# Kernel tuning notes

Hardware: AMD Instinct MI355X
Metric: run time of the kernel (lower is better)

Reference implementation:

```python
import jax, jax.numpy as jnp
import numpy as np

N, M, D, H = 256, 1024, 512, 512


def setup_inputs() -> dict:
    key = jax.random.key(0)
    k1, k2, k3, k4 = jax.random.split(key, 4)
    scale = 1.0 / np.sqrt(D)
    return {
        "embeddings": jax.random.normal(k1, (N, D), dtype=jnp.float32),
        "support_tensors": jax.random.normal(k2, (M, D), dtype=jnp.float32),
        "W1": jax.random.normal(k3, (D, H), dtype=jnp.float32) * scale,
        "b1": jnp.zeros((H,), dtype=jnp.float32),
        "W2": jax.random.normal(k4, (H, 1), dtype=jnp.float32) * (1.0 / np.sqrt(H)),
        "b2": jnp.zeros((1,), dtype=jnp.float32),
    }


def reference(embeddings, support_tensors, W1, b1, W2, b2):
    # SupportLayer.call: tile queries x support set into all N*M pairs,
    # apply pairwise kernel (siamese head: sigmoid(MLP(|a - b|))),
    # reshape back to similarity matrix [N, M].
    # Broadcasting replaces the explicit tf.tile / reshape.
    diff = jnp.abs(embeddings[:, None, :] - support_tensors[None, :, :])  # [N, M, D]
    h = jax.nn.relu(jnp.einsum("nmd,dh->nmh", diff, W1) + b1)             # [N, M, H]
    logits = jnp.einsum("nmh,ho->nmo", h, W2)[..., 0] + b2[0]             # [N, M]
    return jax.nn.sigmoid(logits)
```

## Files before the change

### kernel.cpp

```cpp
#include <hip/hip_runtime.h>
#include <hip/hip_bf16.h>

#define N_Q 256
#define M_S 1024
#define DD 512
#define HH 512

typedef __attribute__((ext_vector_type(8))) short short8;
typedef __attribute__((ext_vector_type(8))) __bf16 bf16x8;
typedef __attribute__((ext_vector_type(16))) float f32x16;
typedef __attribute__((ext_vector_type(2))) __bf16 bf16x2;

union U8 { short8 s; bf16x8 b; };

__device__ __forceinline__ unsigned short f2bf(float f) {
  unsigned int u = __float_as_uint(f);
  u += 0x7FFFu + ((u >> 16) & 1u);
  return (unsigned short)(u >> 16);
}

__device__ __forceinline__ short8 pack8(const float* d) {
#if defined(__has_builtin) && __has_builtin(__builtin_amdgcn_cvt_pk_bf16_f32)
  short8 r;
#pragma unroll
  for (int i = 0; i < 4; ++i) {
    union { bf16x2 v; short s[2]; } u;
    u.v = __builtin_amdgcn_cvt_pk_bf16_f32(d[2 * i], d[2 * i + 1]);
    r[2 * i] = u.s[0];
    r[2 * i + 1] = u.s[1];
  }
  return r;
#else
  short8 r;
#pragma unroll
  for (int i = 0; i < 8; ++i) r[i] = (short)f2bf(d[i]);
  return r;
#endif
}

__device__ __forceinline__ short8 packdiff(float4 e0, float4 e1, float4 s0, float4 s1) {
  float d[8];
  d[0] = fabsf(e0.x - s0.x); d[1] = fabsf(e0.y - s0.y);
  d[2] = fabsf(e0.z - s0.z); d[3] = fabsf(e0.w - s0.w);
  d[4] = fabsf(e1.x - s1.x); d[5] = fabsf(e1.y - s1.y);
  d[6] = fabsf(e1.z - s1.z); d[7] = fabsf(e1.w - s1.w);
  return pack8(d);
}

__global__ __launch_bounds__(512) void prep_w1s(const float* __restrict__ W1,
                                                unsigned short* __restrict__ w1s) {
  const int f = blockIdx.x;
  const int kc = f >> 4, h32 = f & 15;
  const int l = threadIdx.x & 63, j = threadIdx.x >> 6;
  const int h = h32 * 32 + (l & 31);
  const int k = kc * 16 + (l >> 5) * 8 + j;
  w1s[f * 512 + l * 8 + j] = f2bf(W1[k * HH + h]);
}

__global__ __launch_bounds__(256, 2) void support_kernel(
    const float* __restrict__ emb, const float* __restrict__ sup,
    const unsigned short* __restrict__ w1s, const float* __restrict__ b1,
    const float* __restrict__ W2, const float* __restrict__ b2,
    float* __restrict__ out) {
  __shared__ short As[64 * 512];

  const int tid = threadIdx.x;
  const int lane = tid & 63;
  const int wid = tid >> 6;
  const int l31 = lane & 31;
  const int khalf = lane >> 5;

  const int m0 = blockIdx.x * 16;
  const int n0 = blockIdx.y * 4;

  {
    const int c = tid & 63;
    const int pg = tid >> 6;
    const float* e = emb + (n0 + pg) * DD + c * 8;
    const float4 e0 = *(const float4*)e;
    const float4 e1 = *(const float4*)(e + 4);
    const float* sp = sup + m0 * DD + c * 8;
#pragma unroll
    for (int j = 0; j < 16; ++j) {
      const float4 s0 = *(const float4*)(sp + j * DD);
      const float4 s1 = *(const float4*)(sp + j * DD + 4);
      const int p = pg * 16 + j;
      *(short8*)&As[p * 512 + ((c ^ (j & 7)) * 8)] = packdiff(e0, e1, s0, s1);
    }
  }
  __syncthreads();

  const unsigned short* bb = w1s + (wid * 4) * 512 + lane * 8;
  const int ar0 = l31 * 512;
  const int ar1 = (32 + l31) * 512;
  const int ax = l31 & 7;

  f32x16 acc[2][4] = {};
  U8 a[2][2], b[2][4];

#pragma unroll
  for (int tj = 0; tj < 4; ++tj) b[0][tj].s = *(const short8*)(bb + tj * 512);
  {
    const int cc = (khalf ^ ax) * 8;
    a[0][0].s = *(const short8*)&As[ar0 + cc];
    a[0][1].s = *(const short8*)&As[ar1 + cc];
  }

#pragma unroll
  for (int kc = 0; kc < 32; ++kc) {
    const int cur = kc & 1, nxt = cur ^ 1;
    if (kc < 31) {
      const unsigned short* bp = bb + (kc + 1) * 16 * 512;
#pragma unroll
      for (int tj = 0; tj < 4; ++tj) b[nxt][tj].s = *(const short8*)(bp + tj * 512);
      const int cc = ((((kc + 1) * 2 + khalf)) ^ ax) * 8;
      a[nxt][0].s = *(const short8*)&As[ar0 + cc];
      a[nxt][1].s = *(const short8*)&As[ar1 + cc];
    }
#pragma unroll
    for (int tj = 0; tj < 4; ++tj) {
      acc[0][tj] = __builtin_amdgcn_mfma_f32_32x32x16_bf16(a[cur][0].b, b[cur][tj].b, acc[0][tj], 0, 0, 0);
      acc[1][tj] = __builtin_amdgcn_mfma_f32_32x32x16_bf16(a[cur][1].b, b[cur][tj].b, acc[1][tj], 0, 0, 0);
    }
  }

  float b1v[4], w2v[4];
#pragma unroll
  for (int tj = 0; tj < 4; ++tj) {
    const int h = wid * 128 + tj * 32 + l31;
    b1v[tj] = b1[h];
    w2v[tj] = W2[h];
  }
  __syncthreads();
  float* psums = (float*)As;
#pragma unroll
  for (int am = 0; am < 2; ++am) {
#pragma unroll
    for (int r = 0; r < 16; ++r) {
      float s = 0.f;
#pragma unroll
      for (int tj = 0; tj < 4; ++tj)
        s += fmaxf(acc[am][tj][r] + b1v[tj], 0.f) * w2v[tj];
      s += __shfl_xor(s, 1, 64);
      s += __shfl_xor(s, 2, 64);
      s += __shfl_xor(s, 4, 64);
      s += __shfl_xor(s, 8, 64);
      s += __shfl_xor(s, 16, 64);
      if (l31 == 0) {
        const int row32 = (r & 3) + 8 * (r >> 2) + 4 * khalf;
        psums[(am * 32 + row32) * 4 + wid] = s;
      }
    }
  }
  __syncthreads();
  if (tid < 64) {
    float t = psums[tid * 4] + psums[tid * 4 + 1] +
              psums[tid * 4 + 2] + psums[tid * 4 + 3] + b2[0];
    out[(n0 + (tid >> 4)) * M_S + m0 + (tid & 15)] = 1.f / (1.f + __expf(-t));
  }
}

extern "C" void kernel_launch(void* const* d_in, const int* in_sizes, int n_in,
                              void* d_out, int out_size, void* d_ws, size_t ws_size,
                              hipStream_t stream) {
  const float* emb = (const float*)d_in[0];
  const float* sup = (const float*)d_in[1];
  const float* W1  = (const float*)d_in[2];
  const float* b1  = (const float*)d_in[3];
  const float* W2  = (const float*)d_in[4];
  const float* b2  = (const float*)d_in[5];
  float* out = (float*)d_out;
  unsigned short* w1s = (unsigned short*)d_ws;

  prep_w1s<<<512, 512, 0, stream>>>(W1, w1s);
  support_kernel<<<dim3(M_S / 16, N_Q / 4), 256, 0, stream>>>(
      emb, sup, w1s, b1, W2, b2, out);
}
```

Baseline: 231.2 us.

## Retile to 128 pairs x 256 hidden per block, split H across grid with atomics

```diff
diff --git a/kernel.cpp b/kernel.cpp
--- a/kernel.cpp
+++ b/kernel.cpp
@@ -60,87 +60,96 @@
 __global__ __launch_bounds__(256, 2) void support_kernel(
     const float* __restrict__ emb, const float* __restrict__ sup,
     const unsigned short* __restrict__ w1s, const float* __restrict__ b1,
-    const float* __restrict__ W2, const float* __restrict__ b2,
-    float* __restrict__ out) {
-  __shared__ short As[64 * 512];
+    const float* __restrict__ W2, float* __restrict__ out) {
+  __shared__ short As[128 * 256];
 
   const int tid = threadIdx.x;
   const int lane = tid & 63;
   const int wid = tid >> 6;
   const int l31 = lane & 31;
   const int khalf = lane >> 5;
+  const int ax = l31 & 7;
 
   const int m0 = blockIdx.x * 16;
-  const int n0 = blockIdx.y * 4;
+  const int n0 = blockIdx.y * 8;
+  const int hz8 = blockIdx.z * 8;
 
-  {
-    const int c = tid & 63;
-    const int pg = tid >> 6;
-    const float* e = emb + (n0 + pg) * DD + c * 8;
-    const float4 e0 = *(const float4*)e;
-    const float4 e1 = *(const float4*)(e + 4);
-    const float* sp = sup + m0 * DD + c * 8;
-#pragma unroll
-    for (int j = 0; j < 16; ++j) {
-      const float4 s0 = *(const float4*)(sp + j * DD);
-      const float4 s1 = *(const float4*)(sp + j * DD + 4);
-      const int p = pg * 16 + j;
-      *(short8*)&As[p * 512 + ((c ^ (j & 7)) * 8)] = packdiff(e0, e1, s0, s1);
-    }
-  }
-  __syncthreads();
+  const unsigned short* bb = w1s + (hz8 + wid * 2) * 512 + lane * 8;
 
-  const unsigned short* bb = w1s + (wid * 4) * 512 + lane * 8;
-  const int ar0 = l31 * 512;
-  const int ar1 = (32 + l31) * 512;
-  const int ax = l31 & 7;
+  const int c = tid & 31;
+  const int nl = tid >> 5;
+  const float* ep_ = emb + (n0 + nl) * DD + c * 8;
+  const float* sp_ = sup + m0 * DD + c * 8;
 
-  f32x16 acc[2][4] = {};
-  U8 a[2][2], b[2][4];
+  f32x16 acc[4][2] = {};
+  U8 a[2][4], b[3][2];
 
 #pragma unroll
-  for (int tj = 0; tj < 4; ++tj) b[0][tj].s = *(const short8*)(bb + tj * 512);
-  {
-    const int cc = (khalf ^ ax) * 8;
-    a[0][0].s = *(const short8*)&As[ar0 + cc];
-    a[0][1].s = *(const short8*)&As[ar1 + cc];
+  for (int tj = 0; tj < 2; ++tj) {
+    b[0][tj].s = *(const short8*)(bb + (0 * 16 + tj) * 512);
+    b[1][tj].s = *(const short8*)(bb + (1 * 16 + tj) * 512);
   }
 
 #pragma unroll
-  for (int kc = 0; kc < 32; ++kc) {
-    const int cur = kc & 1, nxt = cur ^ 1;
-    if (kc < 31) {
-      const unsigned short* bp = bb + (kc + 1) * 16 * 512;
+  for (int half = 0; half < 2; ++half) {
+    {
+      const float4 e0 = *(const float4*)(ep_ + half * 256);
+      const float4 e1 = *(const float4*)(ep_ + half * 256 + 4);
 #pragma unroll
-      for (int tj = 0; tj < 4; ++tj) b[nxt][tj].s = *(const short8*)(bp + tj * 512);
-      const int cc = ((((kc + 1) * 2 + khalf)) ^ ax) * 8;
-      a[nxt][0].s = *(const short8*)&As[ar0 + cc];
-      a[nxt][1].s = *(const short8*)&As[ar1 + cc];
+      for (int m = 0; m < 16; ++m) {
+        const float* sp = sp_ + m * DD + half * 256;
+        const float4 s0 = *(const float4*)sp;
+        const float4 s1 = *(const float4*)(sp + 4);
+        const int p = nl * 16 + m;
+        *(short8*)&As[p * 256 + ((c ^ (m & 7)) * 8)] = packdiff(e0, e1, s0, s1);
+      }
     }
+    __syncthreads();
+
 #pragma unroll
-    for (int tj = 0; tj < 4; ++tj) {
-      acc[0][tj] = __builtin_amdgcn_mfma_f32_32x32x16_bf16(a[cur][0].b, b[cur][tj].b, acc[0][tj], 0, 0, 0);
-      acc[1][tj] = __builtin_amdgcn_mfma_f32_32x32x16_bf16(a[cur][1].b, b[cur][tj].b, acc[1][tj], 0, 0, 0);
+    for (int am = 0; am < 4; ++am)
+      a[0][am].s = *(const short8*)&As[(am * 32 + l31) * 256 + ((khalf ^ ax) * 8)];
+
+#pragma unroll
+    for (int kc = 0; kc < 16; ++kc) {
+      const int ks = half * 16 + kc;
+      const int cur = kc & 1, nxt = cur ^ 1;
+      if (kc < 15) {
+        const int cc = (((kc + 1) * 2 + khalf) ^ ax) * 8;
+#pragma unroll
+        for (int am = 0; am < 4; ++am)
+          a[nxt][am].s = *(const short8*)&As[(am * 32 + l31) * 256 + cc];
+      }
+      if (ks + 2 < 32) {
+#pragma unroll
+        for (int tj = 0; tj < 2; ++tj)
+          b[(ks + 2) % 3][tj].s = *(const short8*)(bb + ((ks + 2) * 16 + tj) * 512);
+      }
+#pragma unroll
+      for (int am = 0; am < 4; ++am)
+#pragma unroll
+        for (int tj = 0; tj < 2; ++tj)
+          acc[am][tj] = __builtin_amdgcn_mfma_f32_32x32x16_bf16(
+              a[cur][am].b, b[ks % 3][tj].b, acc[am][tj], 0, 0, 0);
     }
+    if (half == 0) __syncthreads();
   }
 
-  float b1v[4], w2v[4];
+  float b1v[2], w2v[2];
 #pragma unroll
-  for (int tj = 0; tj < 4; ++tj) {
-    const int h = wid * 128 + tj * 32 + l31;
+  for (int tj = 0; tj < 2; ++tj) {
+    const int h = (hz8 + wid * 2 + tj) * 32 + l31;
     b1v[tj] = b1[h];
     w2v[tj] = W2[h];
   }
   __syncthreads();
   float* psums = (float*)As;
 #pragma unroll
-  for (int am = 0; am < 2; ++am) {
+  for (int am = 0; am < 4; ++am) {
 #pragma unroll
     for (int r = 0; r < 16; ++r) {
-      float s = 0.f;
-#pragma unroll
-      for (int tj = 0; tj < 4; ++tj)
-        s += fmaxf(acc[am][tj][r] + b1v[tj], 0.f) * w2v[tj];
+      float s = fmaxf(acc[am][0][r] + b1v[0], 0.f) * w2v[0] +
+                fmaxf(acc[am][1][r] + b1v[1], 0.f) * w2v[1];
       s += __shfl_xor(s, 1, 64);
       s += __shfl_xor(s, 2, 64);
       s += __shfl_xor(s, 4, 64);
@@ -153,11 +162,18 @@
     }
   }
   __syncthreads();
-  if (tid < 64) {
-    float t = psums[tid * 4] + psums[tid * 4 + 1] +
-              psums[tid * 4 + 2] + psums[tid * 4 + 3] + b2[0];
-    out[(n0 + (tid >> 4)) * M_S + m0 + (tid & 15)] = 1.f / (1.f + __expf(-t));
+  if (tid < 128) {
+    const float v = psums[tid * 4] + psums[tid * 4 + 1] +
+                    psums[tid * 4 + 2] + psums[tid * 4 + 3];
+    atomicAdd(out + (n0 + (tid >> 4)) * M_S + m0 + (tid & 15), v);
   }
+}
+
+__global__ __launch_bounds__(256) void logits_finalize(float* __restrict__ out,
+                                                       const float* __restrict__ b2) {
+  const int i = blockIdx.x * 256 + threadIdx.x;
+  const float t = out[i] + b2[0];
+  out[i] = 1.f / (1.f + __expf(-t));
 }
 
 extern "C" void kernel_launch(void* const* d_in, const int* in_sizes, int n_in,
@@ -173,6 +189,8 @@
   unsigned short* w1s = (unsigned short*)d_ws;
 
   prep_w1s<<<512, 512, 0, stream>>>(W1, w1s);
-  support_kernel<<<dim3(M_S / 16, N_Q / 4), 256, 0, stream>>>(
-      emb, sup, w1s, b1, W2, b2, out);
+  hipMemsetAsync(d_out, 0, (size_t)N_Q * M_S * sizeof(float), stream);
+  support_kernel<<<dim3(M_S / 16, N_Q / 8, 2), 256, 0, stream>>>(
+      emb, sup, w1s, b1, W2, out);
+  logits_finalize<<<(N_Q * M_S) / 256, 256, 0, stream>>>(out, b2);
 }
```

After: 279.4 us. 1.21x slower.
